# Kernel optimization log

Measured on AMD Instinct MI355X. Metric: run time of the kernel, lower is better.

The kernel has to match this reference:

```python
import jax, jax.numpy as jnp
import numpy as np

N = 50000          # nodes
E = 400000         # edges
F = 128            # num_embeddings
NUM_TYPES = 100    # num_atoms (embedding vocab)
CUTOFF = 5.0
N_RBF = 20


def _silu(x):
    return x * jax.nn.sigmoid(x)


def setup_inputs() -> dict:
    key = jax.random.key(0)
    ks = jax.random.split(key, 16)
    pos = jax.random.normal(ks[0], (N, 3), dtype=jnp.float32) * 3.0
    z = jax.random.randint(ks[1], (N,), 0, NUM_TYPES)
    dst = jax.random.randint(ks[2], (E,), 0, N)
    # ensure src != dst so distances are nonzero
    src = (dst + 1 + jax.random.randint(ks[3], (E,), 0, N - 1)) % N
    def lin(k, fan_in, fan_out):
        kw, kb = jax.random.split(k)
        lim = 1.0 / np.sqrt(fan_in)
        W = jax.random.uniform(kw, (fan_out, fan_in), minval=-lim, maxval=lim, dtype=jnp.float32)
        b = jax.random.uniform(kb, (fan_out,), minval=-lim, maxval=lim, dtype=jnp.float32)
        return W, b
    emb_table = jax.random.normal(ks[4], (NUM_TYPES, F), dtype=jnp.float32)
    Wp1, bp1 = lin(ks[5], F, F)
    Wp2, bp2 = lin(ks[6], F, 3 * F)
    Ww, bw = lin(ks[7], N_RBF, 3 * F)
    Wu, bu = lin(ks[8], F, F)
    Wv, bv = lin(ks[9], F, F)
    Wu1, bu1 = lin(ks[10], 2 * F, F)
    Wu2, bu2 = lin(ks[11], F, 3 * F)
    return dict(pos=pos, emb_table=emb_table,
                Wp1=Wp1, bp1=bp1, Wp2=Wp2, bp2=bp2, Ww=Ww, bw=bw,
                Wu=Wu, bu=bu, Wv=Wv, bv=bv, Wu1=Wu1, bu1=bu1, Wu2=Wu2, bu2=bu2,
                z=z, src=src, dst=dst)


def painn_forward(pos, emb_table, Wp1, bp1, Wp2, bp2, Ww, bw, Wu, bu, Wv, bv,
                  Wu1, bu1, Wu2, bu2, z, src, dst):
    s = emb_table[z]                                  # [N,F] scalar features
    v = jnp.zeros((N, F, 3), dtype=s.dtype)          # equivariant features

    # ---- message block ----
    phi = _silu(s @ Wp1.T + bp1) @ Wp2.T + bp2       # [N,3F]
    rel = pos[dst] - pos[src]                        # [E,3]
    d = jnp.maximum(jnp.linalg.norm(rel, axis=-1), 1e-9)  # [E]
    n = jnp.arange(1, N_RBF + 1, dtype=jnp.float32)
    rbf = jnp.sin(n * jnp.pi * d[:, None] / CUTOFF) / d[:, None]   # [E,20]
    Wf = rbf @ Ww.T + bw                             # [E,3F]
    split = phi[src] * Wf                            # [E,3F] gated message
    ds = jax.ops.segment_sum(split[:, :F], dst, num_segments=N)    # [N,F]
    direction = rel / d[:, None]                     # [E,3]
    dv_e = v[src] * split[:, F:2 * F, None] + split[:, 2 * F:, None] * direction[:, None, :]  # [E,F,3]
    dv = jax.ops.segment_sum(dv_e, dst, num_segments=N)            # [N,F,3]
    s = s + ds
    v = v + dv

    # ---- update block ----
    U = jnp.einsum('nfc,gf->ngc', v, Wu) + bu[:, None]   # [N,F,3]
    V = jnp.einsum('nfc,gf->ngc', v, Wv) + bv[:, None]   # [N,F,3]
    Vn = jnp.linalg.norm(V, axis=-1)                     # [N,F]
    h = jnp.concatenate([s, Vn], axis=-1)                # [N,2F]
    a = _silu(h @ Wu1.T + bu1) @ Wu2.T + bu2             # [N,3F]
    dv2 = U * a[:, :F, None]                             # [N,F,3]
    ds2 = a[:, F:2 * F] + jnp.sum(U * V, axis=-1) * a[:, 2 * F:]   # [N,F]
    return s + ds2, v + dv2


def reference(pos, emb_table, Wp1, bp1, Wp2, bp2, Ww, bw, Wu, bu, Wv, bv,
              Wu1, bu1, Wu2, bu2, z, src, dst):
    return painn_forward(pos, emb_table, Wp1, bp1, Wp2, bp2, Ww, bw, Wu, bu,
                         Wv, bv, Wu1, bu1, Wu2, bu2, z, src, dst)
```

## Files before the change

### kernel.cpp

```cpp
#include <hip/hip_runtime.h>

#define NN 50000
#define EE 400000
#define FF 128
#define NRBF 20
#define MAXDEG 64
#define PI_OVER_CUT 0.6283185307179586f

typedef _Float16 h8 __attribute__((ext_vector_type(8)));
typedef float    f4 __attribute__((ext_vector_type(4)));

union pk32 { unsigned int u; _Float16 h[2]; };

__global__ __launch_bounds__(256) void k_zero(int* __restrict__ counts) {
    int i = blockIdx.x * 256 + threadIdx.x;
    if (i < NN) counts[i] = 0;
}

__global__ __launch_bounds__(256) void k_bucket(const int* __restrict__ dst,
                                                int* __restrict__ counts,
                                                int* __restrict__ slots) {
    int e = blockIdx.x * 256 + threadIdx.x;
    if (e < EE) {
        int n = dst[e];
        int slot = atomicAdd(&counts[n], 1);
        if (slot < MAXDEG) slots[n * MAXDEG + slot] = e;
    }
}

__global__ __launch_bounds__(256) void k_wconv(
    const float* __restrict__ Wu, const float* __restrict__ Wv,
    const float* __restrict__ Wu1, const float* __restrict__ Wu2,
    const float* __restrict__ Wp1, const float* __restrict__ Wp2,
    const float* __restrict__ Ww, const float* __restrict__ bw,
    _Float16* __restrict__ Wuh, _Float16* __restrict__ Wvh,
    _Float16* __restrict__ Wu1h, _Float16* __restrict__ Wu2h,
    _Float16* __restrict__ Wp1h, _Float16* __restrict__ Wp2h,
    _Float16* __restrict__ Wwh32)
{
    int i = blockIdx.x * 256 + threadIdx.x;
    if (i < 16384) { Wuh[i] = (_Float16)Wu[i]; Wvh[i] = (_Float16)Wv[i];
                     Wp1h[i] = (_Float16)Wp1[i]; }
    if (i < 32768) { Wu1h[i] = (_Float16)Wu1[i]; }
    if (i < 49152) { Wu2h[i] = (_Float16)Wu2[i]; Wp2h[i] = (_Float16)Wp2[i]; }
    if (i < 8192) {
        int col = i >> 5, k = i & 31;
        int sr = col < 128 ? col : col + 128;
        _Float16 v = (_Float16)0.f;
        if (k < 20)       v = (_Float16)Ww[sr * NRBF + k];
        else if (k == 20) v = (_Float16)bw[sr];
        Wwh32[i] = v;
    }
}

__global__ __launch_bounds__(256) void k_node_phi_mfma(
    const float* __restrict__ emb, const int* __restrict__ z,
    const _Float16* __restrict__ Wp1h, const float* __restrict__ bp1,
    const _Float16* __restrict__ Wp2h, const float* __restrict__ bp2,
    unsigned int* __restrict__ phi_pk, float* __restrict__ s_io)
{
    __shared__ _Float16 Ss[32 * 128];
    __shared__ _Float16 H1s[32 * 128];

    const int t    = threadIdx.x;
    const int lane = t & 63;
    const int w    = t >> 6;
    const int lr   = lane & 15;
    const int lq   = lane >> 4;
    const int n0   = blockIdx.x * 32;
    const f4 z4 = {0.f, 0.f, 0.f, 0.f};

    for (int i = t; i < 512; i += 256) {
        int n = i >> 4, gr = i & 15;
        int nn = n0 + n; if (nn > NN - 1) nn = NN - 1;
        const float* sp = &emb[(size_t)z[nn] * FF + gr * 8];
        float4 aa = *(const float4*)sp;
        float4 bb = *(const float4*)(sp + 4);
        h8 hv;
        hv[0] = (_Float16)aa.x; hv[1] = (_Float16)aa.y;
        hv[2] = (_Float16)aa.z; hv[3] = (_Float16)aa.w;
        hv[4] = (_Float16)bb.x; hv[5] = (_Float16)bb.y;
        hv[6] = (_Float16)bb.z; hv[7] = (_Float16)bb.w;
        *(h8*)&Ss[(n * 16 + (gr ^ (n & 15))) * 8] = hv;
        float* op = &s_io[(size_t)nn * FF + gr * 8];
        *(float4*)op       = aa;
        *(float4*)(op + 4) = bb;
    }
    __syncthreads();

    f4 acc1[2][2];
    #pragma unroll
    for (int a = 0; a < 2; ++a)
        #pragma unroll
        for (int m = 0; m < 2; ++m) acc1[a][m] = z4;
    {
        const _Float16* bb = Wp1h + (size_t)lr * 128 + lq * 8;
        #pragma unroll
        for (int g2 = 0; g2 < 2; ++g2) {
            h8 bf[4];
            #pragma unroll
            for (int ks = 0; ks < 4; ++ks)
                bf[ks] = *(const h8*)(bb + ((2 * w + g2) * 16) * 128 + ks * 32);
            #pragma unroll
            for (int mt = 0; mt < 2; ++mt) {
                const int r = mt * 16 + lr;
                #pragma unroll
                for (int ks = 0; ks < 4; ++ks) {
                    h8 af = *(const h8*)&Ss[(r * 16 + ((ks * 4 + lq) ^ (r & 15))) * 8];
                    acc1[g2][mt] = __builtin_amdgcn_mfma_f32_16x16x32_f16(
                        af, bf[ks], acc1[g2][mt], 0, 0, 0);
                }
            }
        }
    }
    #pragma unroll
    for (int g2 = 0; g2 < 2; ++g2) {
        const int g = (2 * w + g2) * 16 + lr;
        const float b1 = bp1[g];
        #pragma unroll
        for (int mt = 0; mt < 2; ++mt)
            #pragma unroll
            for (int r = 0; r < 4; ++r) {
                float x = acc1[g2][mt][r] + b1;
                float y = x / (1.f + __expf(-x));
                int n = mt * 16 + lq * 4 + r;
                H1s[(n * 16 + ((g >> 3) ^ (n & 15))) * 8 + (g & 7)] = (_Float16)y;
            }
    }
    __syncthreads();

    f4 accS[2][2], accV[2][2];
    #pragma unroll
    for (int a = 0; a < 2; ++a)
        #pragma unroll
        for (int m = 0; m < 2; ++m) { accS[a][m] = z4; accV[a][m] = z4; }
    {
        const _Float16* bbs = Wp2h + (size_t)lr * 128 + lq * 8;
        const _Float16* bbv = Wp2h + (size_t)(256 + lr) * 128 + lq * 8;
        #pragma unroll
        for (int g2 = 0; g2 < 2; ++g2) {
            h8 bfs[4], bfv[4];
            #pragma unroll
            for (int ks = 0; ks < 4; ++ks) {
                bfs[ks] = *(const h8*)(bbs + ((2 * w + g2) * 16) * 128 + ks * 32);
                bfv[ks] = *(const h8*)(bbv + ((2 * w + g2) * 16) * 128 + ks * 32);
            }
            #pragma unroll
            for (int mt = 0; mt < 2; ++mt) {
                const int r = mt * 16 + lr;
                #pragma unroll
                for (int ks = 0; ks < 4; ++ks) {
                    h8 af = *(const h8*)&H1s[(r * 16 + ((ks * 4 + lq) ^ (r & 15))) * 8];
                    accS[g2][mt] = __builtin_amdgcn_mfma_f32_16x16x32_f16(
                        af, bfs[ks], accS[g2][mt], 0, 0, 0);
                    accV[g2][mt] = __builtin_amdgcn_mfma_f32_16x16x32_f16(
                        af, bfv[ks], accV[g2][mt], 0, 0, 0);
                }
            }
        }
    }
    #pragma unroll
    for (int g2 = 0; g2 < 2; ++g2) {
        const int g = (2 * w + g2) * 16 + lr;
        const float bsa = bp2[g], bva = bp2[256 + g];
        #pragma unroll
        for (int mt = 0; mt < 2; ++mt)
            #pragma unroll
            for (int r = 0; r < 4; ++r) {
                int n = mt * 16 + lq * 4 + r;
                int nn = n0 + n;
                if (nn < NN) {
                    pk32 pk;
                    pk.h[0] = (_Float16)(accS[g2][mt][r] + bsa);
                    pk.h[1] = (_Float16)(accV[g2][mt][r] + bva);
                    phi_pk[(size_t)nn * FF + g] = pk.u;
                }
            }
    }
}

__global__ __launch_bounds__(128) void k_edge_mfma(
    const float* __restrict__ pos,
    const _Float16* __restrict__ Wwh32,
    const int* __restrict__ src,
    const int* __restrict__ counts, const int* __restrict__ slots,
    const unsigned int* __restrict__ phi_pk,
    float* __restrict__ s_io, float* __restrict__ v_io,
    _Float16* __restrict__ xg)
{
    __shared__ _Float16 A[16 * 32];
    __shared__ float dirs[16][4];
    __shared__ float dls[16];
    __shared__ unsigned int wf[16 * 130];

    const int t    = threadIdx.x;
    const int lane = t & 63;
    const int w    = t >> 6;
    const int lr   = lane & 15;
    const int lq   = lane >> 4;
    const int n    = blockIdx.x;
    const f4 z4 = {0.f, 0.f, 0.f, 0.f};

    h8 bf[8];
    #pragma unroll
    for (int j = 0; j < 8; ++j)
        bf[j] = *(const h8*)&Wwh32[(size_t)((w * 8 + j) * 16 + lr) * 32 + lq * 8];

    const float px = pos[3 * n], py = pos[3 * n + 1], pz = pos[3 * n + 2];

    int deg = counts[n];
    deg = deg > MAXDEG ? MAXDEG : deg;

    float acc_s = 0.f, av0 = 0.f, av1 = 0.f, av2 = 0.f;

    for (int t0 = 0; t0 < deg; t0 += 16) {
        const int degT = (deg - t0) < 16 ? (deg - t0) : 16;
        __syncthreads();
        if (t < degT) {
            int e  = slots[n * MAXDEG + t0 + t];
            int sI = src[e];
            float rx = px - pos[3 * sI];
            float ry = py - pos[3 * sI + 1];
            float rz = pz - pos[3 * sI + 2];
            float d = sqrtf(rx * rx + ry * ry + rz * rz);
            d = fmaxf(d, 1e-9f);
            float di = 1.f / d;
            dirs[t][0] = rx * di;
            dirs[t][1] = ry * di;
            dirs[t][2] = rz * di;
            dirs[t][3] = __int_as_float(sI);
            dls[t] = d;
        }
        __syncthreads();
        {
            const int m = t & 15, kk = t >> 4;
            float d  = dls[m];
            float di = 1.f / d;
            float v0 = __sinf((float)(kk + 1) * PI_OVER_CUT * d) * di;
            float v1 = __sinf((float)(kk + 9) * PI_OVER_CUT * d) * di;
            float v2;
            if (kk < 4)       v2 = __sinf((float)(kk + 17) * PI_OVER_CUT * d) * di;
            else if (kk == 4) v2 = 1.0f;
            else              v2 = 0.f;
            #define STO(K, V) A[m * 32 + (((K) >> 3) ^ (m & 3)) * 8 + ((K) & 7)] = (_Float16)(V)
            STO(kk,      v0);
            STO(kk + 8,  v1);
            STO(kk + 16, v2);
            STO(kk + 24, 0.f);
            #undef STO
        }
        __syncthreads();
        {
            h8 af = *(const h8*)&A[(lr * 4 + (lq ^ (lr & 3))) * 8];
            #pragma unroll
            for (int j = 0; j < 8; ++j) {
                f4 dd = __builtin_amdgcn_mfma_f32_16x16x32_f16(af, bf[j], z4, 0, 0, 0);
                #pragma unroll
                for (int r = 0; r < 4; ++r) {
                    int m = lq * 4 + r;
                    ((_Float16*)&wf[m * 130 + j * 16 + lr])[w] = (_Float16)dd[r];
                }
            }
        }
        __syncthreads();
        for (int m = 0; m < degT; ++m) {
            float4 dir = *(const float4*)&dirs[m][0];
            int sI = __builtin_amdgcn_readfirstlane(__float_as_int(dir.w));
            pk32 ph, wfu;
            ph.u  = phi_pk[(size_t)sI * FF + t];
            wfu.u = wf[m * 130 + t];
            float ps = (float)ph.h[0] * (float)wfu.h[0];
            float pv = (float)ph.h[1] * (float)wfu.h[1];
            acc_s += ps;
            av0 = fmaf(pv, dir.x, av0);
            av1 = fmaf(pv, dir.y, av1);
            av2 = fmaf(pv, dir.z, av2);
        }
    }

    size_t gi = (size_t)n * FF + t;
    s_io[gi] += acc_s;
    v_io[gi * 3 + 0] = av0;
    v_io[gi * 3 + 1] = av1;
    v_io[gi * 3 + 2] = av2;
    xg[((size_t)n * 3 + 0) * FF + t] = (_Float16)av0;
    xg[((size_t)n * 3 + 1) * FF + t] = (_Float16)av1;
    xg[((size_t)n * 3 + 2) * FF + t] = (_Float16)av2;
}

__global__ __launch_bounds__(256) void k_update_mfma(
    const _Float16* __restrict__ xg,
    const _Float16* __restrict__ Wuh, const _Float16* __restrict__ Wvh,
    const _Float16* __restrict__ Wu1h, const _Float16* __restrict__ Wu2h,
    const float* __restrict__ bu, const float* __restrict__ bv,
    const float* __restrict__ bu1, const float* __restrict__ bu2,
    float* __restrict__ s_io, float* __restrict__ v_io)
{
    __shared__ _Float16 Xs[96 * 128];
    __shared__ _Float16 Hs[32 * 256];
    __shared__ _Float16 H1s[32 * 128];

    const int t    = threadIdx.x;
    const int lane = t & 63;
    const int w    = t >> 6;
    const int lr   = lane & 15;
    const int lq   = lane >> 4;
    const int n0   = blockIdx.x * 32;
    const f4 z4 = {0.f, 0.f, 0.f, 0.f};

    for (int i = t; i < 1536; i += 256) {
        int row = i >> 4, gr = i & 15;
        int n = row & 31, c = row >> 5;
        int nn = n0 + n; if (nn > NN - 1) nn = NN - 1;
        uint4 d = *(const uint4*)&xg[((size_t)nn * 3 + c) * FF + gr * 8];
        *(uint4*)&Xs[(row * 16 + (gr ^ (row & 15))) * 8] = d;
    }
    for (int i = t; i < 512; i += 256) {
        int n = i >> 4, gr = i & 15;
        int nn = n0 + n; if (nn > NN - 1) nn = NN - 1;
        const float* sp = &s_io[(size_t)nn * FF + gr * 8];
        float4 aa = *(const float4*)sp;
        float4 bb = *(const float4*)(sp + 4);
        h8 hv;
        hv[0] = (_Float16)aa.x; hv[1] = (_Float16)aa.y;
        hv[2] = (_Float16)aa.z; hv[3] = (_Float16)aa.w;
        hv[4] = (_Float16)bb.x; hv[5] = (_Float16)bb.y;
        hv[6] = (_Float16)bb.z; hv[7] = (_Float16)bb.w;
        *(h8*)&Hs[(n * 32 + (gr ^ (n & 15))) * 8] = hv;
    }
    __syncthreads();

    f4 accU[2][6], accV[2][6];
    #pragma unroll
    for (int a = 0; a < 2; ++a)
        #pragma unroll
        for (int m = 0; m < 6; ++m) { accU[a][m] = z4; accV[a][m] = z4; }

    {
        const _Float16* bb = Wuh + (size_t)lr * 128 + lq * 8;
        h8 bfr[2][4];
        #pragma unroll
        for (int g2 = 0; g2 < 2; ++g2)
            #pragma unroll
            for (int ks = 0; ks < 4; ++ks)
                bfr[g2][ks] = *(const h8*)(bb + ((2 * w + g2) * 16) * 128 + ks * 32);
        #pragma unroll
        for (int mt = 0; mt < 6; ++mt) {
            const int r = mt * 16 + lr;
            h8 af[4];
            #pragma unroll
            for (int ks = 0; ks < 4; ++ks)
                af[ks] = *(const h8*)&Xs[(r * 16 + ((ks * 4 + lq) ^ (r & 15))) * 8];
            #pragma unroll
            for (int g2 = 0; g2 < 2; ++g2)
                #pragma unroll
                for (int ks = 0; ks < 4; ++ks)
                    accU[g2][mt] = __builtin_amdgcn_mfma_f32_16x16x32_f16(
                        af[ks], bfr[g2][ks], accU[g2][mt], 0, 0, 0);
        }
    }
    {
        const _Float16* bb = Wvh + (size_t)lr * 128 + lq * 8;
        h8 bfr[2][4];
        #pragma unroll
        for (int g2 = 0; g2 < 2; ++g2)
            #pragma unroll
            for (int ks = 0; ks < 4; ++ks)
                bfr[g2][ks] = *(const h8*)(bb + ((2 * w + g2) * 16) * 128 + ks * 32);
        #pragma unroll
        for (int mt = 0; mt < 6; ++mt) {
            const int r = mt * 16 + lr;
            h8 af[4];
            #pragma unroll
            for (int ks = 0; ks < 4; ++ks)
                af[ks] = *(const h8*)&Xs[(r * 16 + ((ks * 4 + lq) ^ (r & 15))) * 8];
            #pragma unroll
            for (int g2 = 0; g2 < 2; ++g2)
                #pragma unroll
                for (int ks = 0; ks < 4; ++ks)
                    accV[g2][mt] = __builtin_amdgcn_mfma_f32_16x16x32_f16(
                        af[ks], bfr[g2][ks], accV[g2][mt], 0, 0, 0);
        }
    }

    float uvr[2][2][4];
    #pragma unroll
    for (int g2 = 0; g2 < 2; ++g2) {
        const int g = (2 * w + g2) * 16 + lr;
        const float bU = bu[g], bV = bv[g];
        #pragma unroll
        for (int p = 0; p < 2; ++p) {
            #pragma unroll
            for (int r = 0; r < 4; ++r) {
                float Ux = accU[g2][0 + p][r] + bU;
                float Uy = accU[g2][2 + p][r] + bU;
                float Uz = accU[g2][4 + p][r] + bU;
                float Vx = accV[g2][0 + p][r] + bV;
                float Vy = accV[g2][2 + p][r] + bV;
                float Vz = accV[g2][4 + p][r] + bV;
                accU[g2][0 + p][r] = Ux;
                accU[g2][2 + p][r] = Uy;
                accU[g2][4 + p][r] = Uz;
                uvr[g2][p][r] = Ux * Vx + Uy * Vy + Uz * Vz;
                float vn = sqrtf(Vx * Vx + Vy * Vy + Vz * Vz);
                int n = p * 16 + lq * 4 + r;
                int gr = 16 + (g >> 3);
                Hs[(n * 32 + (gr ^ (n & 15))) * 8 + (g & 7)] = (_Float16)vn;
            }
        }
    }
    __syncthreads();

    f4 acc2[2][2];
    #pragma unroll
    for (int a = 0; a < 2; ++a)
        #pragma unroll
        for (int m = 0; m < 2; ++m) acc2[a][m] = z4;
    {
        const _Float16* bb = Wu1h + (size_t)lr * 256 + lq * 8;
        #pragma unroll
        for (int g2 = 0; g2 < 2; ++g2) {
            h8 bfr[8];
            #pragma unroll
            for (int ks = 0; ks < 8; ++ks)
                bfr[ks] = *(const h8*)(bb + ((2 * w + g2) * 16) * 256 + ks * 32);
            #pragma unroll
            for (int mt = 0; mt < 2; ++mt) {
                const int r = mt * 16 + lr;
                #pragma unroll
                for (int ks = 0; ks < 8; ++ks) {
                    h8 af = *(const h8*)&Hs[(r * 32 + ((ks * 4 + lq) ^ (r & 15))) * 8];
                    acc2[g2][mt] = __builtin_amdgcn_mfma_f32_16x16x32_f16(
                        af, bfr[ks], acc2[g2][mt], 0, 0, 0);
                }
            }
        }
    }
    #pragma unroll
    for (int g2 = 0; g2 < 2; ++g2) {
        const int g = (2 * w + g2) * 16 + lr;
        const float b1 = bu1[g];
        #pragma unroll
        for (int mt = 0; mt < 2; ++mt)
            #pragma unroll
            for (int r = 0; r < 4; ++r) {
                float x = acc2[g2][mt][r] + b1;
                float y = x / (1.f + __expf(-x));
                int n = mt * 16 + lq * 4 + r;
                int gr = g >> 3;
                H1s[(n * 16 + (gr ^ (n & 15))) * 8 + (g & 7)] = (_Float16)y;
            }
    }
    __syncthreads();

    f4 acc3[3][2][2];
    #pragma unroll
    for (int a = 0; a < 3; ++a)
        #pragma unroll
        for (int b = 0; b < 2; ++b)
            #pragma unroll
            for (int m = 0; m < 2; ++m) acc3[a][b][m] = z4;
    {
        const _Float16* bb = Wu2h + (size_t)lr * 128 + lq * 8;
        #pragma unroll
        for (int ai = 0; ai < 3; ++ai)
            #pragma unroll
            for (int g2 = 0; g2 < 2; ++g2) {
                const int jt = ai * 8 + 2 * w + g2;
                h8 bfr[4];
                #pragma unroll
                for (int ks = 0; ks < 4; ++ks)
                    bfr[ks] = *(const h8*)(bb + (size_t)(jt * 16) * 128 + ks * 32);
                #pragma unroll
                for (int mt = 0; mt < 2; ++mt) {
                    const int r = mt * 16 + lr;
                    #pragma unroll
                    for (int ks = 0; ks < 4; ++ks) {
                        h8 af = *(const h8*)&H1s[(r * 16 + ((ks * 4 + lq) ^ (r & 15))) * 8];
                        acc3[ai][g2][mt] = __builtin_amdgcn_mfma_f32_16x16x32_f16(
                            af, bfr[ks], acc3[ai][g2][mt], 0, 0, 0);
                    }
                }
            }
    }

    #pragma unroll
    for (int g2 = 0; g2 < 2; ++g2) {
        const int g = (2 * w + g2) * 16 + lr;
        const float b1 = bu2[g], b2 = bu2[128 + g], b3 = bu2[256 + g];
        #pragma unroll
        for (int p = 0; p < 2; ++p)
            #pragma unroll
            for (int r = 0; r < 4; ++r) {
                int n = p * 16 + lq * 4 + r;
                int nn = n0 + n;
                if (nn < NN) {
                    float a1 = acc3[0][g2][p][r] + b1;
                    float a2 = acc3[1][g2][p][r] + b2;
                    float a3 = acc3[2][g2][p][r] + b3;
                    size_t gi = (size_t)nn * FF + g;
                    s_io[gi] += a2 + uvr[g2][p][r] * a3;
                    v_io[gi * 3 + 0] += accU[g2][0 + p][r] * a1;
                    v_io[gi * 3 + 1] += accU[g2][2 + p][r] * a1;
                    v_io[gi * 3 + 2] += accU[g2][4 + p][r] * a1;
                }
            }
    }
}

extern "C" void kernel_launch(void* const* d_in, const int* in_sizes, int n_in,
                              void* d_out, int out_size, void* d_ws, size_t ws_size,
                              hipStream_t stream)
{
    const float* pos = (const float*)d_in[0];
    const float* emb = (const float*)d_in[1];
    const float* Wp1 = (const float*)d_in[2];
    const float* bp1 = (const float*)d_in[3];
    const float* Wp2 = (const float*)d_in[4];
    const float* bp2 = (const float*)d_in[5];
    const float* Ww  = (const float*)d_in[6];
    const float* bw  = (const float*)d_in[7];
    const float* Wu  = (const float*)d_in[8];
    const float* bu  = (const float*)d_in[9];
    const float* Wv  = (const float*)d_in[10];
    const float* bv  = (const float*)d_in[11];
    const float* Wu1 = (const float*)d_in[12];
    const float* bu1 = (const float*)d_in[13];
    const float* Wu2 = (const float*)d_in[14];
    const float* bu2 = (const float*)d_in[15];
    const int* z   = (const int*)d_in[16];
    const int* src = (const int*)d_in[17];
    const int* dst = (const int*)d_in[18];

    float* s_io = (float*)d_out;
    float* v_io = (float*)d_out + (size_t)NN * FF;

    char* ws = (char*)d_ws;
    unsigned int* phi_pk = (unsigned int*)ws;
    _Float16* xg    = (_Float16*)(phi_pk + (size_t)NN * FF);
    _Float16* Wuh   = xg + (size_t)NN * 3 * FF;
    _Float16* Wvh   = Wuh  + 128 * 128;
    _Float16* Wu1h  = Wvh  + 128 * 128;
    _Float16* Wu2h  = Wu1h + 128 * 256;
    _Float16* Wp1h  = Wu2h + 384 * 128;
    _Float16* Wp2h  = Wp1h + 128 * 128;
    _Float16* Wwh32 = Wp2h + 384 * 128;
    int* counts = (int*)(Wwh32 + 256 * 32);
    int* slots  = counts + NN;

    k_zero  <<<(NN + 255) / 256, 256, 0, stream>>>(counts);
    k_bucket<<<(EE + 255) / 256, 256, 0, stream>>>(dst, counts, slots);
    k_wconv <<<192, 256, 0, stream>>>(Wu, Wv, Wu1, Wu2, Wp1, Wp2, Ww, bw,
                                      Wuh, Wvh, Wu1h, Wu2h, Wp1h, Wp2h, Wwh32);
    k_node_phi_mfma<<<(NN + 31) / 32, 256, 0, stream>>>(emb, z, Wp1h, bp1,
                                                        Wp2h, bp2,
                                                        phi_pk, s_io);
    k_edge_mfma<<<NN, 128, 0, stream>>>(pos, Wwh32, src, counts, slots,
                                        phi_pk, s_io, v_io, xg);
    k_update_mfma<<<(NN + 31) / 32, 256, 0, stream>>>(xg, Wuh, Wvh, Wu1h, Wu2h,
                                                      bu, bv, bu1, bu2, s_io, v_io);
}
```

Measured before the change: 424.9 us.

## Keep intermediate s/v in fp16 workspace and write outputs once in update kernel

The edge kernel no longer writes the fp32 s and v outputs. It keeps the intermediate scalar features in an fp16 buffer and the vector features only in the existing fp16 xg buffer. The update kernel reads these and writes the final s and v once, with no read-modify-write of the fp32 outputs. The update kernel now tiles 16 nodes per block instead of 32, and the counts zeroing is folded into the weight-convert kernel. This cuts global memory traffic and one launch, but the residual s and v now pass through fp16, which lowers precision.

```diff
diff --git a/kernel.cpp b/kernel.cpp
--- a/kernel.cpp
+++ b/kernel.cpp
@@ -11,11 +11,6 @@
 typedef float    f4 __attribute__((ext_vector_type(4)));
 
 union pk32 { unsigned int u; _Float16 h[2]; };
-
-__global__ __launch_bounds__(256) void k_zero(int* __restrict__ counts) {
-    int i = blockIdx.x * 256 + threadIdx.x;
-    if (i < NN) counts[i] = 0;
-}
 
 __global__ __launch_bounds__(256) void k_bucket(const int* __restrict__ dst,
                                                 int* __restrict__ counts,
@@ -36,9 +31,10 @@
     _Float16* __restrict__ Wuh, _Float16* __restrict__ Wvh,
     _Float16* __restrict__ Wu1h, _Float16* __restrict__ Wu2h,
     _Float16* __restrict__ Wp1h, _Float16* __restrict__ Wp2h,
-    _Float16* __restrict__ Wwh32)
+    _Float16* __restrict__ Wwh32, int* __restrict__ counts)
 {
     int i = blockIdx.x * 256 + threadIdx.x;
+    if (i < NN) counts[i] = 0;
     if (i < 16384) { Wuh[i] = (_Float16)Wu[i]; Wvh[i] = (_Float16)Wv[i];
                      Wp1h[i] = (_Float16)Wp1[i]; }
     if (i < 32768) { Wu1h[i] = (_Float16)Wu1[i]; }
@@ -57,7 +53,7 @@
     const float* __restrict__ emb, const int* __restrict__ z,
     const _Float16* __restrict__ Wp1h, const float* __restrict__ bp1,
     const _Float16* __restrict__ Wp2h, const float* __restrict__ bp2,
-    unsigned int* __restrict__ phi_pk, float* __restrict__ s_io)
+    unsigned int* __restrict__ phi_pk, _Float16* __restrict__ s_h)
 {
     __shared__ _Float16 Ss[32 * 128];
     __shared__ _Float16 H1s[32 * 128];
@@ -82,9 +78,7 @@
         hv[4] = (_Float16)bb.x; hv[5] = (_Float16)bb.y;
         hv[6] = (_Float16)bb.z; hv[7] = (_Float16)bb.w;
         *(h8*)&Ss[(n * 16 + (gr ^ (n & 15))) * 8] = hv;
-        float* op = &s_io[(size_t)nn * FF + gr * 8];
-        *(float4*)op       = aa;
-        *(float4*)(op + 4) = bb;
+        *(h8*)&s_h[(size_t)nn * FF + gr * 8] = hv;
     }
     __syncthreads();
 
@@ -185,7 +179,7 @@
     const int* __restrict__ src,
     const int* __restrict__ counts, const int* __restrict__ slots,
     const unsigned int* __restrict__ phi_pk,
-    float* __restrict__ s_io, float* __restrict__ v_io,
+    _Float16* __restrict__ s_h,
     _Float16* __restrict__ xg)
 {
     __shared__ _Float16 A[16 * 32];
@@ -279,62 +273,53 @@
     }
 
     size_t gi = (size_t)n * FF + t;
-    s_io[gi] += acc_s;
-    v_io[gi * 3 + 0] = av0;
-    v_io[gi * 3 + 1] = av1;
-    v_io[gi * 3 + 2] = av2;
+    float s_old = (float)s_h[gi];
+    s_h[gi] = (_Float16)(s_old + acc_s);
     xg[((size_t)n * 3 + 0) * FF + t] = (_Float16)av0;
     xg[((size_t)n * 3 + 1) * FF + t] = (_Float16)av1;
     xg[((size_t)n * 3 + 2) * FF + t] = (_Float16)av2;
 }
 
 __global__ __launch_bounds__(256) void k_update_mfma(
-    const _Float16* __restrict__ xg,
+    const _Float16* __restrict__ xg, const _Float16* __restrict__ s_h,
     const _Float16* __restrict__ Wuh, const _Float16* __restrict__ Wvh,
     const _Float16* __restrict__ Wu1h, const _Float16* __restrict__ Wu2h,
     const float* __restrict__ bu, const float* __restrict__ bv,
     const float* __restrict__ bu1, const float* __restrict__ bu2,
     float* __restrict__ s_io, float* __restrict__ v_io)
 {
-    __shared__ _Float16 Xs[96 * 128];
-    __shared__ _Float16 Hs[32 * 256];
-    __shared__ _Float16 H1s[32 * 128];
+    __shared__ _Float16 Xs[48 * 128];
+    __shared__ _Float16 Hs[16 * 256];
+    __shared__ _Float16 H1s[16 * 128];
 
     const int t    = threadIdx.x;
     const int lane = t & 63;
     const int w    = t >> 6;
     const int lr   = lane & 15;
     const int lq   = lane >> 4;
-    const int n0   = blockIdx.x * 32;
+    const int n0   = blockIdx.x * 16;
     const f4 z4 = {0.f, 0.f, 0.f, 0.f};
 
-    for (int i = t; i < 1536; i += 256) {
+    for (int i = t; i < 768; i += 256) {
         int row = i >> 4, gr = i & 15;
-        int n = row & 31, c = row >> 5;
+        int n = row & 15, c = row >> 4;
         int nn = n0 + n; if (nn > NN - 1) nn = NN - 1;
         uint4 d = *(const uint4*)&xg[((size_t)nn * 3 + c) * FF + gr * 8];
-        *(uint4*)&Xs[(row * 16 + (gr ^ (row & 15))) * 8] = d;
-    }
-    for (int i = t; i < 512; i += 256) {
-        int n = i >> 4, gr = i & 15;
+        *(uint4*)&Xs[(row * 16 + (gr ^ n)) * 8] = d;
+    }
+    {
+        int n = t >> 4, gr = t & 15;
         int nn = n0 + n; if (nn > NN - 1) nn = NN - 1;
-        const float* sp = &s_io[(size_t)nn * FF + gr * 8];
-        float4 aa = *(const float4*)sp;
-        float4 bb = *(const float4*)(sp + 4);
-        h8 hv;
-        hv[0] = (_Float16)aa.x; hv[1] = (_Float16)aa.y;
-        hv[2] = (_Float16)aa.z; hv[3] = (_Float16)aa.w;
-        hv[4] = (_Float16)bb.x; hv[5] = (_Float16)bb.y;
-        hv[6] = (_Float16)bb.z; hv[7] = (_Float16)bb.w;
-        *(h8*)&Hs[(n * 32 + (gr ^ (n & 15))) * 8] = hv;
+        uint4 d = *(const uint4*)&s_h[(size_t)nn * FF + gr * 8];
+        *(uint4*)&Hs[(n * 32 + (gr ^ n)) * 8] = d;
     }
     __syncthreads();
 
-    f4 accU[2][6], accV[2][6];
+    f4 accU[2][3], accV[2][3];
     #pragma unroll
     for (int a = 0; a < 2; ++a)
         #pragma unroll
-        for (int m = 0; m < 6; ++m) { accU[a][m] = z4; accV[a][m] = z4; }
+        for (int c = 0; c < 3; ++c) { accU[a][c] = z4; accV[a][c] = z4; }
 
     {
         const _Float16* bb = Wuh + (size_t)lr * 128 + lq * 8;
@@ -345,18 +330,18 @@
             for (int ks = 0; ks < 4; ++ks)
                 bfr[g2][ks] = *(const h8*)(bb + ((2 * w + g2) * 16) * 128 + ks * 32);
         #pragma unroll
-        for (int mt = 0; mt < 6; ++mt) {
-            const int r = mt * 16 + lr;
+        for (int c = 0; c < 3; ++c) {
+            const int rr = c * 16 + lr;
             h8 af[4];
             #pragma unroll
             for (int ks = 0; ks < 4; ++ks)
-                af[ks] = *(const h8*)&Xs[(r * 16 + ((ks * 4 + lq) ^ (r & 15))) * 8];
+                af[ks] = *(const h8*)&Xs[(rr * 16 + ((ks * 4 + lq) ^ lr)) * 8];
             #pragma unroll
             for (int g2 = 0; g2 < 2; ++g2)
                 #pragma unroll
                 for (int ks = 0; ks < 4; ++ks)
-                    accU[g2][mt] = __builtin_amdgcn_mfma_f32_16x16x32_f16(
-                        af[ks], bfr[g2][ks], accU[g2][mt], 0, 0, 0);
+                    accU[g2][c] = __builtin_amdgcn_mfma_f32_16x16x32_f16(
+                        af[ks], bfr[g2][ks], accU[g2][c], 0, 0, 0);
         }
     }
     {
@@ -368,54 +353,48 @@
             for (int ks = 0; ks < 4; ++ks)
                 bfr[g2][ks] = *(const h8*)(bb + ((2 * w + g2) * 16) * 128 + ks * 32);
         #pragma unroll
-        for (int mt = 0; mt < 6; ++mt) {
-            const int r = mt * 16 + lr;
+        for (int c = 0; c < 3; ++c) {
+            const int rr = c * 16 + lr;
             h8 af[4];
             #pragma unroll
             for (int ks = 0; ks < 4; ++ks)
-                af[ks] = *(const h8*)&Xs[(r * 16 + ((ks * 4 + lq) ^ (r & 15))) * 8];
+                af[ks] = *(const h8*)&Xs[(rr * 16 + ((ks * 4 + lq) ^ lr)) * 8];
             #pragma unroll
             for (int g2 = 0; g2 < 2; ++g2)
                 #pragma unroll
                 for (int ks = 0; ks < 4; ++ks)
-                    accV[g2][mt] = __builtin_amdgcn_mfma_f32_16x16x32_f16(
-                        af[ks], bfr[g2][ks], accV[g2][mt], 0, 0, 0);
-        }
-    }
-
-    float uvr[2][2][4];
+                    accV[g2][c] = __builtin_amdgcn_mfma_f32_16x16x32_f16(
+                        af[ks], bfr[g2][ks], accV[g2][c], 0, 0, 0);
+        }
+    }
+
+    float uvr[2][4];
     #pragma unroll
     for (int g2 = 0; g2 < 2; ++g2) {
         const int g = (2 * w + g2) * 16 + lr;
         const float bU = bu[g], bV = bv[g];
         #pragma unroll
-        for (int p = 0; p < 2; ++p) {
-            #pragma unroll
-            for (int r = 0; r < 4; ++r) {
-                float Ux = accU[g2][0 + p][r] + bU;
-                float Uy = accU[g2][2 + p][r] + bU;
-                float Uz = accU[g2][4 + p][r] + bU;
-                float Vx = accV[g2][0 + p][r] + bV;
-                float Vy = accV[g2][2 + p][r] + bV;
-                float Vz = accV[g2][4 + p][r] + bV;
-                accU[g2][0 + p][r] = Ux;
-                accU[g2][2 + p][r] = Uy;
-                accU[g2][4 + p][r] = Uz;
-                uvr[g2][p][r] = Ux * Vx + Uy * Vy + Uz * Vz;
-                float vn = sqrtf(Vx * Vx + Vy * Vy + Vz * Vz);
-                int n = p * 16 + lq * 4 + r;
-                int gr = 16 + (g >> 3);
-                Hs[(n * 32 + (gr ^ (n & 15))) * 8 + (g & 7)] = (_Float16)vn;
-            }
+        for (int r = 0; r < 4; ++r) {
+            float Ux = accU[g2][0][r] + bU;
+            float Uy = accU[g2][1][r] + bU;
+            float Uz = accU[g2][2][r] + bU;
+            float Vx = accV[g2][0][r] + bV;
+            float Vy = accV[g2][1][r] + bV;
+            float Vz = accV[g2][2][r] + bV;
+            accU[g2][0][r] = Ux;
+            accU[g2][1][r] = Uy;
+            accU[g2][2][r] = Uz;
+            uvr[g2][r] = Ux * Vx + Uy * Vy + Uz * Vz;
+            float vn = sqrtf(Vx * Vx + Vy * Vy + Vz * Vz);
+            int n = lq * 4 + r;
+            int gr = 16 + (g >> 3);
+            Hs[(n * 32 + (gr ^ n)) * 8 + (g & 7)] = (_Float16)vn;
         }
     }
     __syncthreads();
 
-    f4 acc2[2][2];
-    #pragma unroll
-    for (int a = 0; a < 2; ++a)
-        #pragma unroll
-        for (int m = 0; m < 2; ++m) acc2[a][m] = z4;
+    f4 acc2[2];
+    acc2[0] = z4; acc2[1] = z4;
     {
         const _Float16* bb = Wu1h + (size_t)lr * 256 + lq * 8;
         #pragma unroll
@@ -425,14 +404,10 @@
             for (int ks = 0; ks < 8; ++ks)
                 bfr[ks] = *(const h8*)(bb + ((2 * w + g2) * 16) * 256 + ks * 32);
             #pragma unroll
-            for (int mt = 0; mt < 2; ++mt) {
-                const int r = mt * 16 + lr;
-                #pragma unroll
-                for (int ks = 0; ks < 8; ++ks) {
-                    h8 af = *(const h8*)&Hs[(r * 32 + ((ks * 4 + lq) ^ (r & 15))) * 8];
-                    acc2[g2][mt] = __builtin_amdgcn_mfma_f32_16x16x32_f16(
-                        af, bfr[ks], acc2[g2][mt], 0, 0, 0);
-                }
+            for (int ks = 0; ks < 8; ++ks) {
+                h8 af = *(const h8*)&Hs[(lr * 32 + ((ks * 4 + lq) ^ lr)) * 8];
+                acc2[g2] = __builtin_amdgcn_mfma_f32_16x16x32_f16(
+                    af, bfr[ks], acc2[g2], 0, 0, 0);
             }
         }
     }
@@ -441,25 +416,18 @@
         const int g = (2 * w + g2) * 16 + lr;
         const float b1 = bu1[g];
         #pragma unroll
-        for (int mt = 0; mt < 2; ++mt)
-            #pragma unroll
-            for (int r = 0; r < 4; ++r) {
-                float x = acc2[g2][mt][r] + b1;
-                float y = x / (1.f + __expf(-x));
-                int n = mt * 16 + lq * 4 + r;
-                int gr = g >> 3;
-                H1s[(n * 16 + (gr ^ (n & 15))) * 8 + (g & 7)] = (_Float16)y;
-            }
+        for (int r = 0; r < 4; ++r) {
+            float x = acc2[g2][r] + b1;
+            float y = x / (1.f + __expf(-x));
+            int n = lq * 4 + r;
+            H1s[(n * 16 + ((g >> 3) ^ n)) * 8 + (g & 7)] = (_Float16)y;
+        }
     }
     __syncthreads();
 
-    f4 acc3[3][2][2];
-    #pragma unroll
-    for (int a = 0; a < 3; ++a)
-        #pragma unroll
-        for (int b = 0; b < 2; ++b)
-            #pragma unroll
-            for (int m = 0; m < 2; ++m) acc3[a][b][m] = z4;
+    f4 acc3[3][2];
+    #pragma unroll
+    for (int a = 0; a < 3; ++a) { acc3[a][0] = z4; acc3[a][1] = z4; }
     {
         const _Float16* bb = Wu2h + (size_t)lr * 128 + lq * 8;
         #pragma unroll
@@ -472,14 +440,10 @@
                 for (int ks = 0; ks < 4; ++ks)
                     bfr[ks] = *(const h8*)(bb + (size_t)(jt * 16) * 128 + ks * 32);
                 #pragma unroll
-                for (int mt = 0; mt < 2; ++mt) {
-                    const int r = mt * 16 + lr;
-                    #pragma unroll
-                    for (int ks = 0; ks < 4; ++ks) {
-                        h8 af = *(const h8*)&H1s[(r * 16 + ((ks * 4 + lq) ^ (r & 15))) * 8];
-                        acc3[ai][g2][mt] = __builtin_amdgcn_mfma_f32_16x16x32_f16(
-                            af, bfr[ks], acc3[ai][g2][mt], 0, 0, 0);
-                    }
+                for (int ks = 0; ks < 4; ++ks) {
+                    h8 af = *(const h8*)&H1s[(lr * 16 + ((ks * 4 + lq) ^ lr)) * 8];
+                    acc3[ai][g2] = __builtin_amdgcn_mfma_f32_16x16x32_f16(
+                        af, bfr[ks], acc3[ai][g2], 0, 0, 0);
                 }
             }
     }
@@ -489,22 +453,24 @@
         const int g = (2 * w + g2) * 16 + lr;
         const float b1 = bu2[g], b2 = bu2[128 + g], b3 = bu2[256 + g];
         #pragma unroll
-        for (int p = 0; p < 2; ++p)
-            #pragma unroll
-            for (int r = 0; r < 4; ++r) {
-                int n = p * 16 + lq * 4 + r;
-                int nn = n0 + n;
-                if (nn < NN) {
-                    float a1 = acc3[0][g2][p][r] + b1;
-                    float a2 = acc3[1][g2][p][r] + b2;
-                    float a3 = acc3[2][g2][p][r] + b3;
-                    size_t gi = (size_t)nn * FF + g;
-                    s_io[gi] += a2 + uvr[g2][p][r] * a3;
-                    v_io[gi * 3 + 0] += accU[g2][0 + p][r] * a1;
-                    v_io[gi * 3 + 1] += accU[g2][2 + p][r] * a1;
-                    v_io[gi * 3 + 2] += accU[g2][4 + p][r] * a1;
-                }
-            }
+        for (int r = 0; r < 4; ++r) {
+            int n = lq * 4 + r;
+            int nn = n0 + n;
+            if (nn < NN) {
+                float a1 = acc3[0][g2][r] + b1;
+                float a2 = acc3[1][g2][r] + b2;
+                float a3 = acc3[2][g2][r] + b3;
+                size_t gi = (size_t)nn * FF + g;
+                float s1 = (float)Hs[(n * 32 + ((g >> 3) ^ n)) * 8 + (g & 7)];
+                s_io[gi] = s1 + a2 + uvr[g2][r] * a3;
+                float vx = (float)Xs[((0 * 16 + n) * 16 + ((g >> 3) ^ n)) * 8 + (g & 7)];
+                float vy = (float)Xs[((1 * 16 + n) * 16 + ((g >> 3) ^ n)) * 8 + (g & 7)];
+                float vz = (float)Xs[((2 * 16 + n) * 16 + ((g >> 3) ^ n)) * 8 + (g & 7)];
+                v_io[gi * 3 + 0] = vx + accU[g2][0][r] * a1;
+                v_io[gi * 3 + 1] = vy + accU[g2][1][r] * a1;
+                v_io[gi * 3 + 2] = vz + accU[g2][2][r] * a1;
+            }
+        }
     }
 }
 
@@ -538,7 +504,8 @@
     char* ws = (char*)d_ws;
     unsigned int* phi_pk = (unsigned int*)ws;
     _Float16* xg    = (_Float16*)(phi_pk + (size_t)NN * FF);
-    _Float16* Wuh   = xg + (size_t)NN * 3 * FF;
+    _Float16* s_h   = xg + (size_t)NN * 3 * FF;
+    _Float16* Wuh   = s_h + (size_t)NN * FF;
     _Float16* Wvh   = Wuh  + 128 * 128;
     _Float16* Wu1h  = Wvh  + 128 * 128;
     _Float16* Wu2h  = Wu1h + 128 * 256;
@@ -548,15 +515,17 @@
     int* counts = (int*)(Wwh32 + 256 * 32);
     int* slots  = counts + NN;
 
-    k_zero  <<<(NN + 255) / 256, 256, 0, stream>>>(counts);
+    k_wconv <<<196, 256, 0, stream>>>(Wu, Wv, Wu1, Wu2, Wp1, Wp2, Ww, bw,
+                                      Wuh, Wvh, Wu1h, Wu2h, Wp1h, Wp2h, Wwh32,
+                                      counts);
     k_bucket<<<(EE + 255) / 256, 256, 0, stream>>>(dst, counts, slots);
-    k_wconv <<<192, 256, 0, stream>>>(Wu, Wv, Wu1, Wu2, Wp1, Wp2, Ww, bw,
-                                      Wuh, Wvh, Wu1h, Wu2h, Wp1h, Wp2h, Wwh32);
     k_node_phi_mfma<<<(NN + 31) / 32, 256, 0, stream>>>(emb, z, Wp1h, bp1,
                                                         Wp2h, bp2,
-                                                        phi_pk, s_io);
+                                                        phi_pk, s_h);
     k_edge_mfma<<<NN, 128, 0, stream>>>(pos, Wwh32, src, counts, slots,
-                                        phi_pk, s_io, v_io, xg);
-    k_update_mfma<<<(NN + 31) / 32, 256, 0, stream>>>(xg, Wuh, Wvh, Wu1h, Wu2h,
-                                                      bu, bv, bu1, bu2, s_io, v_io);
+                                        phi_pk, s_h, xg);
+    k_update_mfma<<<(NN + 15) / 16, 256, 0, stream>>>(xg, s_h,
+                                                      Wuh, Wvh, Wu1h, Wu2h,
+                                                      bu, bv, bu1, bu2,
+                                                      s_io, v_io);
 }
```

Measured after the change: 388.5 us. 8.6% less time.
